# Kernel optimization log

Measured on AMD Instinct MI355X. Metric: run time of the kernel, lower is better.

## Reference

```python
import jax, jax.numpy as jnp
import numpy as np

N_QUBITS = 10
Q_DEPTH = 6


def _apply_1q(state, gate, wire):
    """Apply a 2x2 gate (or batched [B,2,2] gates) to `wire` of state [B,2,...,2]."""
    s = jnp.moveaxis(state, wire + 1, -1)
    if gate.ndim == 2:
        s = s @ gate.T  # new_j = sum_i G[j,i] * old_i
    else:
        s = jnp.einsum('b...i,bji->b...j', s, gate)
    return jnp.moveaxis(s, -1, wire + 1)


def _apply_cnot(state, ctrl, tgt):
    s = jnp.moveaxis(state, (ctrl + 1, tgt + 1), (-2, -1))
    s = jnp.stack([s[..., 0, :], s[..., 1, ::-1]], axis=-2)  # flip target where ctrl=1
    return jnp.moveaxis(s, (-2, -1), (ctrl + 1, tgt + 1))


def _ry(theta):
    """RY(theta) = [[cos(t/2), -sin(t/2)], [sin(t/2), cos(t/2)]]; theta scalar or [B]."""
    c, s = jnp.cos(theta / 2.0), jnp.sin(theta / 2.0)
    return jnp.stack([jnp.stack([c, -s], -1), jnp.stack([s, c], -1)], -2)


def _vqc(angles, q_weights):
    """angles: [B, n_qubits] per-sample RY angles; q_weights: [q_depth, n_qubits].
    Returns <PauliZ_w> for every wire: [B, n_qubits]. All gates are real -> float32 state."""
    B, n = angles.shape
    q_depth = q_weights.shape[0]
    # H-layer on |0...0> gives the uniform superposition: all amplitudes 2^{-n/2}
    state = jnp.full((B,) + (2,) * n, 2.0 ** (-n / 2.0), dtype=angles.dtype)
    # RY layer with per-sample input angles
    for w in range(n):
        state = _apply_1q(state, _ry(angles[:, w]), w)
    # q_depth x (brick-wall CNOT entangler + trainable RY layer)
    for k in range(q_depth):
        for i in range(0, n - 1, 2):
            state = _apply_cnot(state, i, i + 1)
        for i in range(1, n - 1, 2):
            state = _apply_cnot(state, i, i + 1)
        for w in range(n):
            state = _apply_1q(state, _ry(q_weights[k, w]), w)
    # expval(PauliZ(w)) = P(wire w = 0) - P(wire w = 1)
    probs = state * state  # real statevector
    exps = []
    for w in range(n):
        p = jnp.moveaxis(probs, w + 1, 1).reshape(B, 2, -1).sum(-1)
        exps.append(p[:, 0] - p[:, 1])
    return jnp.stack(exps, -1)


def setup_inputs() -> dict:
    key = jax.random.key(0)
    ks = jax.random.split(key, 6)
    B, D_IN, OUT = 8192, 512, 64
    x = jax.random.normal(ks[0], (B, D_IN), dtype=jnp.float32)
    W1 = jax.random.normal(ks[1], (D_IN, N_QUBITS), dtype=jnp.float32) * (1.0 / np.sqrt(D_IN))
    b1 = jnp.zeros((N_QUBITS,), dtype=jnp.float32)
    # keras 'uniform' initializer: U(-0.05, 0.05)
    q_weights = jax.random.uniform(ks[2], (Q_DEPTH, N_QUBITS), dtype=jnp.float32,
                                   minval=-0.05, maxval=0.05)
    W2 = jax.random.normal(ks[3], (N_QUBITS, OUT), dtype=jnp.float32) * (1.0 / np.sqrt(N_QUBITS))
    b2 = jnp.zeros((OUT,), dtype=jnp.float32)
    return {"x": x, "W1": W1, "b1": b1, "q_weights": q_weights, "W2": W2, "b2": b2}


def reference(x, W1, b1, q_weights, W2, b2):
    # Dense(n_qubits, tanh) then scale to angles in (-pi/2, pi/2)
    angles = jnp.tanh(x @ W1 + b1) * (jnp.pi / 2.0)  # [B, n_qubits]
    q_out = _vqc(angles, q_weights)                   # [B, n_qubits]
    return q_out @ W2 + b2                            # [B, output_dim]
```

## Files before the change

### kernel.cpp

```cpp
#include <hip/hip_runtime.h>

#define NQ 10
#define QD 6
#define DIN 512
#define DOUT 64

typedef float v2f __attribute__((ext_vector_type(2)));

__device__ __forceinline__ v2f sp(float s) { v2f r; r.x = s; r.y = s; return r; }
__device__ __forceinline__ v2f mk(float a, float b) { v2f r; r.x = a; r.y = b; return r; }
#define PKF(a, b, c) __builtin_elementwise_fma(a, b, c)

template <int CTRL>
__device__ __forceinline__ float dppf(float v) {
    return __int_as_float(__builtin_amdgcn_mov_dpp(__float_as_int(v), CTRL, 0xF, 0xF, true));
}
template <int M>
__device__ __forceinline__ float sx(float v) {
    if constexpr (M == 1)       return dppf<0xB1>(v);
    else if constexpr (M == 2)  return dppf<0x4E>(v);
    else if constexpr (M == 4)  return dppf<0x1B>(dppf<0x141>(v));
    else if constexpr (M == 8)  return dppf<0x128>(v);
    else return __int_as_float(__builtin_amdgcn_ds_swizzle(__float_as_int(v), 0x401F));
}
template <int M>
__device__ __forceinline__ v2f sx2(v2f v) { return mk(sx<M>(v.x), sx<M>(v.y)); }
__device__ __forceinline__ float red32(float v) {
    v += dppf<0x128>(v);
    v += dppf<0x124>(v);
    v += dppf<0x122>(v);
    v += dppf<0x121>(v);
    v += sx<16>(v);
    return v;
}

__global__ __launch_bounds__(256, 4) void dqc_main(
    const float* __restrict__ x,
    const float* __restrict__ W1,
    const float* __restrict__ b1,
    const float* __restrict__ qw,
    const float* __restrict__ W2,
    const float* __restrict__ b2,
    float* __restrict__ out,
    const int B)
{
    __shared__ __align__(16) float csl[2 * QD * NQ];

    const int tid = threadIdx.x;
    if (tid < QD * NQ) {
        float s, c;
        sincosf(qw[tid] * 0.5f, &s, &c);
        csl[2 * tid] = c; csl[2 * tid + 1] = s;
    }

    const int lane32 = tid & 31;
    const int b  = (blockIdx.x * 256 + tid) >> 5;
    const int bb = (b < B) ? b : (B - 1);

    float xr[16];
    {
        const float4* xp = (const float4*)(x + (size_t)bb * DIN + lane32 * 16);
        #pragma unroll
        for (int i = 0; i < 4; ++i) {
            const float4 v = xp[i];
            xr[4*i] = v.x; xr[4*i+1] = v.y; xr[4*i+2] = v.z; xr[4*i+3] = v.w;
        }
    }
    float dot[NQ];
    #pragma unroll
    for (int w = 0; w < NQ; ++w) dot[w] = 0.f;
    {
        const float4* wp = (const float4*)(W1 + (size_t)lane32 * 16 * NQ);
        #pragma unroll
        for (int j = 0; j < 8; ++j) {
            const float4 f0 = wp[5*j], f1 = wp[5*j+1], f2 = wp[5*j+2],
                         f3 = wp[5*j+3], f4 = wp[5*j+4];
            const float xa = xr[2*j], xb = xr[2*j+1];
            dot[0]=fmaf(xa,f0.x,dot[0]); dot[1]=fmaf(xa,f0.y,dot[1]);
            dot[2]=fmaf(xa,f0.z,dot[2]); dot[3]=fmaf(xa,f0.w,dot[3]);
            dot[4]=fmaf(xa,f1.x,dot[4]); dot[5]=fmaf(xa,f1.y,dot[5]);
            dot[6]=fmaf(xa,f1.z,dot[6]); dot[7]=fmaf(xa,f1.w,dot[7]);
            dot[8]=fmaf(xa,f2.x,dot[8]); dot[9]=fmaf(xa,f2.y,dot[9]);
            dot[0]=fmaf(xb,f2.z,dot[0]); dot[1]=fmaf(xb,f2.w,dot[1]);
            dot[2]=fmaf(xb,f3.x,dot[2]); dot[3]=fmaf(xb,f3.y,dot[3]);
            dot[4]=fmaf(xb,f3.z,dot[4]); dot[5]=fmaf(xb,f3.w,dot[5]);
            dot[6]=fmaf(xb,f4.x,dot[6]); dot[7]=fmaf(xb,f4.y,dot[7]);
            dot[8]=fmaf(xb,f4.z,dot[8]); dot[9]=fmaf(xb,f4.w,dot[9]);
        }
    }
    #pragma unroll
    for (int w = 0; w < NQ; ++w) dot[w] = red32(dot[w]);

    float u0[NQ], u1[NQ];
    #pragma unroll
    for (int w = 0; w < NQ; ++w) {
        const float th2 = tanhf(dot[w] + b1[w]) * 0.78539816339744830962f;
        float s, c;
        sincosf(th2, &s, &c);
        const float isq2 = 0.70710678118654752440f;
        u0[w] = (c - s) * isq2;
        u1[w] = (c + s) * isq2;
    }

    v2f A[16];
    {
        float lf = ((lane32 & 16) ? u1[0] : u0[0]);
        lf *= ((((lane32 >> 3) ^ (lane32 >> 4)) & 1) ? u1[1] : u0[1]);
        lf *= ((lane32 & 4) ? u1[2] : u0[2]);
        lf *= ((((lane32 >> 1) ^ (lane32 >> 2)) & 1) ? u1[3] : u0[3]);
        lf *= ((lane32 & 1) ? u1[4] : u0[4]);
        const bool b0 = (lane32 & 1) != 0;
        const float w5a = b0 ? u1[5] : u0[5];
        const float w5b = b0 ? u0[5] : u1[5];
        #pragma unroll
        for (int m = 0; m < 16; ++m) {
            float f = ((m & 8) ? w5b : w5a);
            f *= ((m & 4) ? u1[6] : u0[6]);
            f *= ((((m >> 1) ^ (m >> 2)) & 1) ? u1[7] : u0[7]);
            f *= ((m & 1) ? u1[8] : u0[8]);
            f *= lf;
            A[m] = (m & 1) ? mk(f * u1[9], f * u0[9]) : mk(f * u0[9], f * u1[9]);
        }
    }

    __syncthreads();

    #pragma unroll 1
    for (int k = 0; k < QD; ++k) {
        const float4* cp = (const float4*)(csl + k * 2 * NQ);
        const float4 g0 = cp[0], g1 = cp[1], g2 = cp[2], g3 = cp[3], g4 = cp[4];
        const float C0=g0.x,S0=g0.y, C1=g0.z,S1=g0.w;
        const float C2=g1.x,S2=g1.y, C3=g1.z,S3=g1.w;
        const float C4=g2.x,S4=g2.y, C5=g2.z,S5=g2.w;
        const float C6=g3.x,S6=g3.y, C7=g3.z,S7=g3.w;
        const float C8=g4.x,S8=g4.y, C9=g4.z,S9=g4.w;
        const bool fuse = (k < QD - 1);

        {
            const float g = (lane32 & 16) ? S0 : -S0;
            const v2f al = sp(C0), be = sp(g);
            #pragma unroll
            for (int m = 0; m < 16; ++m) { const v2f p = sx2<16>(A[m]); A[m] = PKF(al, A[m], be * p); }
        }
        {
            const float g = (lane32 & 4) ? S2 : -S2;
            const bool cb = (lane32 & 8) != 0;
            const v2f al = sp(cb ? g : C2), be = sp(cb ? C2 : g);
            #pragma unroll
            for (int m = 0; m < 16; ++m) { const v2f p = sx2<4>(A[m]); A[m] = PKF(al, A[m], be * p); }
        }
        {
            const float g = (lane32 & 1) ? S4 : -S4;
            const bool cb = (lane32 & 2) != 0;
            const v2f al = sp(cb ? g : C4), be = sp(cb ? C4 : g);
            #pragma unroll
            for (int m = 0; m < 16; ++m) { const v2f p = sx2<1>(A[m]); A[m] = PKF(al, A[m], be * p); }
        }
        {
            #pragma unroll
            for (int m = 0; m < 16; ++m) {
                if (m & 4) continue;
                const v2f lo = A[m], hi = A[m + 4];
                if ((m >> 3) & 1) {
                    A[m]     = PKF(sp(-S6), lo, sp(C6) * hi);
                    A[m + 4] = PKF(sp( S6), hi, sp(C6) * lo);
                } else {
                    A[m]     = PKF(sp(C6), lo, sp(-S6) * hi);
                    A[m + 4] = PKF(sp(C6), hi, sp( S6) * lo);
                }
            }
        }
        {
            #pragma unroll
            for (int m = 0; m < 16; m += 2) {
                const v2f lo = A[m], hi = A[m + 1];
                if ((m >> 1) & 1) {
                    A[m]     = PKF(sp(-S8), lo, sp(C8) * hi);
                    A[m + 1] = PKF(sp( S8), hi, sp(C8) * lo);
                } else {
                    A[m]     = PKF(sp(C8), lo, sp(-S8) * hi);
                    A[m + 1] = PKF(sp(C8), hi, sp( S8) * lo);
                }
            }
        }

        {
            const float g = (lane32 & 8) ? S1 : -S1;
            const bool cb = fuse && ((lane32 & 16) != 0);
            const v2f al = sp(cb ? -g : C1), be = sp(cb ? C1 : g);
            #pragma unroll
            for (int m = 0; m < 16; ++m) { const v2f p = sx2<8>(A[m]); A[m] = PKF(al, A[m], be * p); }
        }
        {
            const float g = (lane32 & 2) ? S3 : -S3;
            const bool cb = fuse && ((lane32 & 4) != 0);
            const v2f al = sp(cb ? -g : C3), be = sp(cb ? C3 : g);
            #pragma unroll
            for (int m = 0; m < 16; ++m) { const v2f p = sx2<2>(A[m]); A[m] = PKF(al, A[m], be * p); }
        }
        {
            const bool cb = fuse && ((lane32 & 1) != 0);
            const v2f a_lo = sp(cb ?  S5 : C5), b_lo = sp(cb ? C5 : -S5);
            const v2f a_hi = sp(cb ? -S5 : C5), b_hi = sp(cb ? C5 :  S5);
            #pragma unroll
            for (int m = 0; m < 8; ++m) {
                const v2f lo = A[m], hi = A[m + 8];
                A[m]     = PKF(a_lo, lo, b_lo * hi);
                A[m + 8] = PKF(a_hi, hi, b_hi * lo);
            }
        }
        {
            #pragma unroll
            for (int m = 0; m < 16; ++m) {
                if (m & 2) continue;
                const v2f lo = A[m], hi = A[m + 2];
                if (fuse && ((m >> 2) & 1)) {
                    A[m]     = PKF(sp( S7), lo, sp(C7) * hi);
                    A[m + 2] = PKF(sp(-S7), hi, sp(C7) * lo);
                } else {
                    A[m]     = PKF(sp(C7), lo, sp(-S7) * hi);
                    A[m + 2] = PKF(sp(C7), hi, sp( S7) * lo);
                }
            }
        }
        {
            const v2f Ae = sp(C9), Be = mk(-S9, S9);
            const v2f Ao = fuse ? mk(S9, -S9) : Ae;
            const v2f Bo = fuse ? sp(C9) : Be;
            #pragma unroll
            for (int m = 0; m < 16; ++m) {
                const v2f s = mk(A[m].y, A[m].x);
                A[m] = (m & 1) ? PKF(Ao, A[m], Bo * s) : PKF(Ae, A[m], Be * s);
            }
        }
    }

    v2f tot2 = sp(0.f), q5 = sp(0.f), q6 = sp(0.f), q7 = sp(0.f), q8 = sp(0.f);
    #pragma unroll
    for (int m = 0; m < 16; ++m) {
        const v2f P = A[m] * A[m];
        tot2 += P;
        if (m & 8) q5 += P;
        if (m & 4) q6 += P;
        if (m & 2) q7 += P;
        if (m & 1) q8 += P;
    }
    const float tot = tot2.x + tot2.y;
    float e[NQ];
    e[0] = (lane32 & 16) ? -tot : tot;
    e[1] = (lane32 & 8)  ? -tot : tot;
    e[2] = (lane32 & 4)  ? -tot : tot;
    e[3] = (lane32 & 2)  ? -tot : tot;
    e[4] = (lane32 & 1)  ? -tot : tot;
    e[5] = tot - 2.f * (q5.x + q5.y);
    e[6] = tot - 2.f * (q6.x + q6.y);
    e[7] = tot - 2.f * (q7.x + q7.y);
    e[8] = tot - 2.f * (q8.x + q8.y);
    e[9] = tot - 2.f * tot2.y;
    #pragma unroll
    for (int w = 0; w < NQ; ++w) e[w] = red32(e[w]);

    if (b < B) {
        float2 o = ((const float2*)b2)[lane32];
        #pragma unroll
        for (int w = 0; w < NQ; ++w) {
            const float2 wv = ((const float2*)(W2 + w * DOUT))[lane32];
            o.x = fmaf(e[w], wv.x, o.x);
            o.y = fmaf(e[w], wv.y, o.y);
        }
        ((float2*)(out + (size_t)b * DOUT))[lane32] = o;
    }
}

extern "C" void kernel_launch(void* const* d_in, const int* in_sizes, int n_in,
                              void* d_out, int out_size, void* d_ws, size_t ws_size,
                              hipStream_t stream) {
    const float* x  = (const float*)d_in[0];
    const float* W1 = (const float*)d_in[1];
    const float* b1 = (const float*)d_in[2];
    const float* qw = (const float*)d_in[3];
    const float* W2 = (const float*)d_in[4];
    const float* b2 = (const float*)d_in[5];
    float* out = (float*)d_out;

    const int B = in_sizes[0] / DIN;
    const int blocks = (B + 7) / 8;
    dqc_main<<<blocks, 256, 0, stream>>>(x, W1, b1, qw, W2, b2, out, B);
}
```

Measured before the change: 108.6 us.

## Spread each sample's statevector across a full 64-lane wavefront instead of 32 lanes

Each sample's 1024-amplitude state now spans 64 lanes with 8 packed pairs per lane instead of 32 lanes with 16 pairs. Wire 0 swaps across the half-wavefront through ds_bpermute, and reductions gain a cross-half step. Gate constants are regrouped in shared memory into even and odd wire sets. The change also uses inline-asm packed FMA/mul/add and doubles the occupancy hint in launch bounds. It halves per-lane register state and work to raise parallelism, at the cost of an LDS-based permute for one wire, a longer reduction and more blocks.

```diff
diff --git a/kernel.cpp b/kernel.cpp
--- a/kernel.cpp
+++ b/kernel.cpp
@@ -9,7 +9,16 @@
 
 __device__ __forceinline__ v2f sp(float s) { v2f r; r.x = s; r.y = s; return r; }
 __device__ __forceinline__ v2f mk(float a, float b) { v2f r; r.x = a; r.y = b; return r; }
-#define PKF(a, b, c) __builtin_elementwise_fma(a, b, c)
+
+__device__ __forceinline__ v2f pk_fma(v2f a, v2f b, v2f c) {
+    v2f d; asm("v_pk_fma_f32 %0, %1, %2, %3" : "=v"(d) : "v"(a), "v"(b), "v"(c)); return d;
+}
+__device__ __forceinline__ v2f pk_mul(v2f a, v2f b) {
+    v2f d; asm("v_pk_mul_f32 %0, %1, %2" : "=v"(d) : "v"(a), "v"(b)); return d;
+}
+__device__ __forceinline__ v2f pk_add(v2f a, v2f b) {
+    v2f d; asm("v_pk_add_f32 %0, %1, %2" : "=v"(d) : "v"(a), "v"(b)); return d;
+}
 
 template <int CTRL>
 __device__ __forceinline__ float dppf(float v) {
@@ -21,20 +30,24 @@
     else if constexpr (M == 2)  return dppf<0x4E>(v);
     else if constexpr (M == 4)  return dppf<0x1B>(dppf<0x141>(v));
     else if constexpr (M == 8)  return dppf<0x128>(v);
-    else return __int_as_float(__builtin_amdgcn_ds_swizzle(__float_as_int(v), 0x401F));
+    else                        return __int_as_float(__builtin_amdgcn_ds_swizzle(__float_as_int(v), 0x401F));
+}
+__device__ __forceinline__ float sx32(float v, int xaddr) {
+    return __int_as_float(__builtin_amdgcn_ds_bpermute(xaddr, __float_as_int(v)));
 }
 template <int M>
 __device__ __forceinline__ v2f sx2(v2f v) { return mk(sx<M>(v.x), sx<M>(v.y)); }
-__device__ __forceinline__ float red32(float v) {
+__device__ __forceinline__ float red64(float v, int xaddr) {
     v += dppf<0x128>(v);
     v += dppf<0x124>(v);
     v += dppf<0x122>(v);
     v += dppf<0x121>(v);
-    v += sx<16>(v);
+    v += __int_as_float(__builtin_amdgcn_ds_swizzle(__float_as_int(v), 0x401F));
+    v += sx32(v, xaddr);
     return v;
 }
 
-__global__ __launch_bounds__(256, 4) void dqc_main(
+__global__ __launch_bounds__(256, 8) void dqc_main(
     const float* __restrict__ x,
     const float* __restrict__ W1,
     const float* __restrict__ b1,
@@ -44,35 +57,36 @@
     float* __restrict__ out,
     const int B)
 {
-    __shared__ __align__(16) float csl[2 * QD * NQ];
+    __shared__ __align__(16) float csl[QD * 24];
 
     const int tid = threadIdx.x;
     if (tid < QD * NQ) {
+        const int layer = tid / NQ, wire = tid - layer * NQ;
         float s, c;
         sincosf(qw[tid] * 0.5f, &s, &c);
-        csl[2 * tid] = c; csl[2 * tid + 1] = s;
-    }
-
-    const int lane32 = tid & 31;
-    const int b  = (blockIdx.x * 256 + tid) >> 5;
+        const int pos = layer * 24 + (wire & 1) * 12 + (wire >> 1) * 2;
+        csl[pos] = c; csl[pos + 1] = s;
+    }
+
+    const int lane = tid & 63;
+    const int b = blockIdx.x * 4 + (tid >> 6);
     const int bb = (b < B) ? b : (B - 1);
-
-    float xr[16];
+    const int xaddr = ((tid ^ 32) & 63) << 2;
+
+    float xr[8];
     {
-        const float4* xp = (const float4*)(x + (size_t)bb * DIN + lane32 * 16);
-        #pragma unroll
-        for (int i = 0; i < 4; ++i) {
-            const float4 v = xp[i];
-            xr[4*i] = v.x; xr[4*i+1] = v.y; xr[4*i+2] = v.z; xr[4*i+3] = v.w;
-        }
+        const float4* xp = (const float4*)(x + (size_t)bb * DIN + lane * 8);
+        const float4 v0 = xp[0], v1 = xp[1];
+        xr[0]=v0.x; xr[1]=v0.y; xr[2]=v0.z; xr[3]=v0.w;
+        xr[4]=v1.x; xr[5]=v1.y; xr[6]=v1.z; xr[7]=v1.w;
     }
     float dot[NQ];
     #pragma unroll
     for (int w = 0; w < NQ; ++w) dot[w] = 0.f;
     {
-        const float4* wp = (const float4*)(W1 + (size_t)lane32 * 16 * NQ);
+        const float4* wp = (const float4*)(W1 + (size_t)lane * 8 * NQ);
         #pragma unroll
-        for (int j = 0; j < 8; ++j) {
+        for (int j = 0; j < 4; ++j) {
             const float4 f0 = wp[5*j], f1 = wp[5*j+1], f2 = wp[5*j+2],
                          f3 = wp[5*j+3], f4 = wp[5*j+4];
             const float xa = xr[2*j], xb = xr[2*j+1];
@@ -89,7 +103,7 @@
         }
     }
     #pragma unroll
-    for (int w = 0; w < NQ; ++w) dot[w] = red32(dot[w]);
+    for (int w = 0; w < NQ; ++w) dot[w] = red64(dot[w], xaddr);
 
     float u0[NQ], u1[NQ];
     #pragma unroll
@@ -102,20 +116,17 @@
         u1[w] = (c + s) * isq2;
     }
 
-    v2f A[16];
+    v2f A[8];
     {
-        float lf = ((lane32 & 16) ? u1[0] : u0[0]);
-        lf *= ((((lane32 >> 3) ^ (lane32 >> 4)) & 1) ? u1[1] : u0[1]);
-        lf *= ((lane32 & 4) ? u1[2] : u0[2]);
-        lf *= ((((lane32 >> 1) ^ (lane32 >> 2)) & 1) ? u1[3] : u0[3]);
-        lf *= ((lane32 & 1) ? u1[4] : u0[4]);
-        const bool b0 = (lane32 & 1) != 0;
-        const float w5a = b0 ? u1[5] : u0[5];
-        const float w5b = b0 ? u0[5] : u1[5];
+        float lf = ((lane & 32) ? u1[0] : u0[0]);
+        lf *= ((((lane >> 4) ^ (lane >> 5)) & 1) ? u1[1] : u0[1]);
+        lf *= ((lane & 8) ? u1[2] : u0[2]);
+        lf *= ((((lane >> 2) ^ (lane >> 3)) & 1) ? u1[3] : u0[3]);
+        lf *= ((lane & 2) ? u1[4] : u0[4]);
+        lf *= (((lane ^ (lane >> 1)) & 1) ? u1[5] : u0[5]);
         #pragma unroll
-        for (int m = 0; m < 16; ++m) {
-            float f = ((m & 8) ? w5b : w5a);
-            f *= ((m & 4) ? u1[6] : u0[6]);
+        for (int m = 0; m < 8; ++m) {
+            float f = ((m & 4) ? u1[6] : u0[6]);
             f *= ((((m >> 1) ^ (m >> 2)) & 1) ? u1[7] : u0[7]);
             f *= ((m & 1) ? u1[8] : u0[8]);
             f *= lf;
@@ -127,148 +138,170 @@
 
     #pragma unroll 1
     for (int k = 0; k < QD; ++k) {
-        const float4* cp = (const float4*)(csl + k * 2 * NQ);
-        const float4 g0 = cp[0], g1 = cp[1], g2 = cp[2], g3 = cp[3], g4 = cp[4];
-        const float C0=g0.x,S0=g0.y, C1=g0.z,S1=g0.w;
-        const float C2=g1.x,S2=g1.y, C3=g1.z,S3=g1.w;
-        const float C4=g2.x,S4=g2.y, C5=g2.z,S5=g2.w;
-        const float C6=g3.x,S6=g3.y, C7=g3.z,S7=g3.w;
-        const float C8=g4.x,S8=g4.y, C9=g4.z,S9=g4.w;
-        const bool fuse = (k < QD - 1);
-
-        {
-            const float g = (lane32 & 16) ? S0 : -S0;
-            const v2f al = sp(C0), be = sp(g);
-            #pragma unroll
-            for (int m = 0; m < 16; ++m) { const v2f p = sx2<16>(A[m]); A[m] = PKF(al, A[m], be * p); }
-        }
-        {
-            const float g = (lane32 & 4) ? S2 : -S2;
-            const bool cb = (lane32 & 8) != 0;
-            const v2f al = sp(cb ? g : C2), be = sp(cb ? C2 : g);
-            #pragma unroll
-            for (int m = 0; m < 16; ++m) { const v2f p = sx2<4>(A[m]); A[m] = PKF(al, A[m], be * p); }
-        }
-        {
-            const float g = (lane32 & 1) ? S4 : -S4;
-            const bool cb = (lane32 & 2) != 0;
-            const v2f al = sp(cb ? g : C4), be = sp(cb ? C4 : g);
-            #pragma unroll
-            for (int m = 0; m < 16; ++m) { const v2f p = sx2<1>(A[m]); A[m] = PKF(al, A[m], be * p); }
-        }
-        {
-            #pragma unroll
-            for (int m = 0; m < 16; ++m) {
-                if (m & 4) continue;
+        const float* ce = csl + k * 24;
+        const bool fuse = (k != QD - 1);
+
+        const float4 ea = *(const float4*)(ce);
+        const float4 eb = *(const float4*)(ce + 4);
+        const float2 ec = *(const float2*)(ce + 8);
+        const float C0=ea.x, S0=ea.y, C2=ea.z, S2=ea.w;
+        const float C4=eb.x, S4=eb.y, C6=eb.z, S6=eb.w;
+        const float C8=ec.x, S8=ec.y;
+
+        {
+            const float g = (lane & 32) ? S0 : -S0;
+            const v2f alv = sp(C0), bev = sp(g);
+            #pragma unroll
+            for (int m = 0; m < 8; ++m) {
+                const v2f p = mk(sx32(A[m].x, xaddr), sx32(A[m].y, xaddr));
+                A[m] = pk_fma(alv, A[m], pk_mul(bev, p));
+            }
+        }
+        {
+            const float g = (lane & 8) ? S2 : -S2;
+            const bool cb = (lane & 16) != 0;
+            const v2f alv = sp(cb ? g : C2), bev = sp(cb ? C2 : g);
+            #pragma unroll
+            for (int m = 0; m < 8; ++m) {
+                const v2f p = sx2<8>(A[m]);
+                A[m] = pk_fma(alv, A[m], pk_mul(bev, p));
+            }
+        }
+        {
+            const float g = (lane & 2) ? S4 : -S4;
+            const bool cb = (lane & 4) != 0;
+            const v2f alv = sp(cb ? g : C4), bev = sp(cb ? C4 : g);
+            #pragma unroll
+            for (int m = 0; m < 8; ++m) {
+                const v2f p = sx2<2>(A[m]);
+                A[m] = pk_fma(alv, A[m], pk_mul(bev, p));
+            }
+        }
+        {
+            const bool cb = (lane & 1) != 0;
+            const v2f a_lo = sp(cb ? -S6 : C6), b_lo = sp(cb ? C6 : -S6);
+            const v2f a_hi = sp(cb ?  S6 : C6), b_hi = sp(cb ? C6 :  S6);
+            #pragma unroll
+            for (int m = 0; m < 4; ++m) {
                 const v2f lo = A[m], hi = A[m + 4];
-                if ((m >> 3) & 1) {
-                    A[m]     = PKF(sp(-S6), lo, sp(C6) * hi);
-                    A[m + 4] = PKF(sp( S6), hi, sp(C6) * lo);
+                A[m]     = pk_fma(a_lo, lo, pk_mul(b_lo, hi));
+                A[m + 4] = pk_fma(a_hi, hi, pk_mul(b_hi, lo));
+            }
+        }
+        {
+            const v2f c8 = sp(C8), s8 = sp(S8), ns8 = sp(-S8);
+            #pragma unroll
+            for (int m = 0; m < 8; m += 2) {
+                const v2f lo = A[m], hi = A[m + 1];
+                if (m & 2) {
+                    A[m]     = pk_fma(ns8, lo, pk_mul(c8, hi));
+                    A[m + 1] = pk_fma(s8,  hi, pk_mul(c8, lo));
                 } else {
-                    A[m]     = PKF(sp(C6), lo, sp(-S6) * hi);
-                    A[m + 4] = PKF(sp(C6), hi, sp( S6) * lo);
+                    A[m]     = pk_fma(c8, lo, pk_mul(ns8, hi));
+                    A[m + 1] = pk_fma(c8, hi, pk_mul(s8,  lo));
                 }
             }
         }
-        {
-            #pragma unroll
-            for (int m = 0; m < 16; m += 2) {
-                const v2f lo = A[m], hi = A[m + 1];
-                if ((m >> 1) & 1) {
-                    A[m]     = PKF(sp(-S8), lo, sp(C8) * hi);
-                    A[m + 1] = PKF(sp( S8), hi, sp(C8) * lo);
+
+        const float4 oa = *(const float4*)(ce + 12);
+        const float4 ob = *(const float4*)(ce + 16);
+        const float2 oc = *(const float2*)(ce + 20);
+        const float C1=oa.x, S1=oa.y, C3=oa.z, S3=oa.w;
+        const float C5=ob.x, S5=ob.y, C7=ob.z, S7=ob.w;
+        const float C9=oc.x, S9=oc.y;
+
+        {
+            const float g = (lane & 16) ? S1 : -S1;
+            const bool cb = fuse && ((lane & 32) != 0);
+            const v2f alv = sp(cb ? -g : C1), bev = sp(cb ? C1 : g);
+            #pragma unroll
+            for (int m = 0; m < 8; ++m) {
+                const v2f p = sx2<16>(A[m]);
+                A[m] = pk_fma(alv, A[m], pk_mul(bev, p));
+            }
+        }
+        {
+            const float g = (lane & 4) ? S3 : -S3;
+            const bool cb = fuse && ((lane & 8) != 0);
+            const v2f alv = sp(cb ? -g : C3), bev = sp(cb ? C3 : g);
+            #pragma unroll
+            for (int m = 0; m < 8; ++m) {
+                const v2f p = sx2<4>(A[m]);
+                A[m] = pk_fma(alv, A[m], pk_mul(bev, p));
+            }
+        }
+        {
+            const float g = (lane & 1) ? S5 : -S5;
+            const bool cb = fuse && ((lane & 2) != 0);
+            const v2f alv = sp(cb ? -g : C5), bev = sp(cb ? C5 : g);
+            #pragma unroll
+            for (int m = 0; m < 8; ++m) {
+                const v2f p = sx2<1>(A[m]);
+                A[m] = pk_fma(alv, A[m], pk_mul(bev, p));
+            }
+        }
+        {
+            const v2f c7 = sp(C7), s7 = sp(S7), ns7 = sp(-S7);
+            const v2f a_lo4 = fuse ? s7 : c7,  b_lo4 = fuse ? c7 : ns7;
+            const v2f a_hi4 = fuse ? ns7 : c7, b_hi4 = fuse ? c7 : s7;
+            #pragma unroll
+            for (int m = 0; m < 2; ++m) {
+                {   const v2f lo = A[m], hi = A[m + 2];
+                    A[m]     = pk_fma(c7, lo, pk_mul(ns7, hi));
+                    A[m + 2] = pk_fma(c7, hi, pk_mul(s7,  lo)); }
+                {   const v2f lo = A[m + 4], hi = A[m + 6];
+                    A[m + 4] = pk_fma(a_lo4, lo, pk_mul(b_lo4, hi));
+                    A[m + 6] = pk_fma(a_hi4, hi, pk_mul(b_hi4, lo)); }
+            }
+        }
+        {
+            const float nS9 = -S9;
+            const float axx = fuse ? S9 : C9,  axy = fuse ? C9 : nS9;
+            const float ayy = fuse ? nS9 : C9, ayx = fuse ? C9 : S9;
+            #pragma unroll
+            for (int m = 0; m < 8; ++m) {
+                const float ax = A[m].x, ay = A[m].y;
+                if (m & 1) {
+                    A[m].x = fmaf(axx, ax, axy * ay);
+                    A[m].y = fmaf(ayy, ay, ayx * ax);
                 } else {
-                    A[m]     = PKF(sp(C8), lo, sp(-S8) * hi);
-                    A[m + 1] = PKF(sp(C8), hi, sp( S8) * lo);
+                    A[m].x = fmaf(C9, ax, nS9 * ay);
+                    A[m].y = fmaf(C9, ay, S9  * ax);
                 }
             }
         }
-
-        {
-            const float g = (lane32 & 8) ? S1 : -S1;
-            const bool cb = fuse && ((lane32 & 16) != 0);
-            const v2f al = sp(cb ? -g : C1), be = sp(cb ? C1 : g);
-            #pragma unroll
-            for (int m = 0; m < 16; ++m) { const v2f p = sx2<8>(A[m]); A[m] = PKF(al, A[m], be * p); }
-        }
-        {
-            const float g = (lane32 & 2) ? S3 : -S3;
-            const bool cb = fuse && ((lane32 & 4) != 0);
-            const v2f al = sp(cb ? -g : C3), be = sp(cb ? C3 : g);
-            #pragma unroll
-            for (int m = 0; m < 16; ++m) { const v2f p = sx2<2>(A[m]); A[m] = PKF(al, A[m], be * p); }
-        }
-        {
-            const bool cb = fuse && ((lane32 & 1) != 0);
-            const v2f a_lo = sp(cb ?  S5 : C5), b_lo = sp(cb ? C5 : -S5);
-            const v2f a_hi = sp(cb ? -S5 : C5), b_hi = sp(cb ? C5 :  S5);
-            #pragma unroll
-            for (int m = 0; m < 8; ++m) {
-                const v2f lo = A[m], hi = A[m + 8];
-                A[m]     = PKF(a_lo, lo, b_lo * hi);
-                A[m + 8] = PKF(a_hi, hi, b_hi * lo);
-            }
-        }
-        {
-            #pragma unroll
-            for (int m = 0; m < 16; ++m) {
-                if (m & 2) continue;
-                const v2f lo = A[m], hi = A[m + 2];
-                if (fuse && ((m >> 2) & 1)) {
-                    A[m]     = PKF(sp( S7), lo, sp(C7) * hi);
-                    A[m + 2] = PKF(sp(-S7), hi, sp(C7) * lo);
-                } else {
-                    A[m]     = PKF(sp(C7), lo, sp(-S7) * hi);
-                    A[m + 2] = PKF(sp(C7), hi, sp( S7) * lo);
-                }
-            }
-        }
-        {
-            const v2f Ae = sp(C9), Be = mk(-S9, S9);
-            const v2f Ao = fuse ? mk(S9, -S9) : Ae;
-            const v2f Bo = fuse ? sp(C9) : Be;
-            #pragma unroll
-            for (int m = 0; m < 16; ++m) {
-                const v2f s = mk(A[m].y, A[m].x);
-                A[m] = (m & 1) ? PKF(Ao, A[m], Bo * s) : PKF(Ae, A[m], Be * s);
-            }
-        }
-    }
-
-    v2f tot2 = sp(0.f), q5 = sp(0.f), q6 = sp(0.f), q7 = sp(0.f), q8 = sp(0.f);
-    #pragma unroll
-    for (int m = 0; m < 16; ++m) {
-        const v2f P = A[m] * A[m];
-        tot2 += P;
-        if (m & 8) q5 += P;
-        if (m & 4) q6 += P;
-        if (m & 2) q7 += P;
-        if (m & 1) q8 += P;
-    }
+    }
+
+    v2f P[8];
+    #pragma unroll
+    for (int m = 0; m < 8; ++m) P[m] = pk_mul(A[m], A[m]);
+    const v2f s01 = pk_add(P[0], P[1]), s23 = pk_add(P[2], P[3]);
+    const v2f s45 = pk_add(P[4], P[5]), s67 = pk_add(P[6], P[7]);
+    const v2f q8v = pk_add(pk_add(P[1], P[3]), pk_add(P[5], P[7]));
+    const v2f q6v = pk_add(s45, s67);
+    const v2f q7v = pk_add(s23, s67);
+    const v2f tot2 = pk_add(pk_add(s01, s23), q6v);
     const float tot = tot2.x + tot2.y;
+
     float e[NQ];
-    e[0] = (lane32 & 16) ? -tot : tot;
-    e[1] = (lane32 & 8)  ? -tot : tot;
-    e[2] = (lane32 & 4)  ? -tot : tot;
-    e[3] = (lane32 & 2)  ? -tot : tot;
-    e[4] = (lane32 & 1)  ? -tot : tot;
-    e[5] = tot - 2.f * (q5.x + q5.y);
-    e[6] = tot - 2.f * (q6.x + q6.y);
-    e[7] = tot - 2.f * (q7.x + q7.y);
-    e[8] = tot - 2.f * (q8.x + q8.y);
-    e[9] = tot - 2.f * tot2.y;
-    #pragma unroll
-    for (int w = 0; w < NQ; ++w) e[w] = red32(e[w]);
+    e[0] = (lane & 32) ? -tot : tot;
+    e[1] = (lane & 16) ? -tot : tot;
+    e[2] = (lane & 8)  ? -tot : tot;
+    e[3] = (lane & 4)  ? -tot : tot;
+    e[4] = (lane & 2)  ? -tot : tot;
+    e[5] = (lane & 1)  ? -tot : tot;
+    e[6] = fmaf(-2.f, q6v.x + q6v.y, tot);
+    e[7] = fmaf(-2.f, q7v.x + q7v.y, tot);
+    e[8] = fmaf(-2.f, q8v.x + q8v.y, tot);
+    e[9] = fmaf(-2.f, tot2.y, tot);
+    #pragma unroll
+    for (int w = 0; w < NQ; ++w) e[w] = red64(e[w], xaddr);
 
     if (b < B) {
-        float2 o = ((const float2*)b2)[lane32];
+        float o = b2[lane];
         #pragma unroll
-        for (int w = 0; w < NQ; ++w) {
-            const float2 wv = ((const float2*)(W2 + w * DOUT))[lane32];
-            o.x = fmaf(e[w], wv.x, o.x);
-            o.y = fmaf(e[w], wv.y, o.y);
-        }
-        ((float2*)(out + (size_t)b * DOUT))[lane32] = o;
+        for (int w = 0; w < NQ; ++w) o = fmaf(e[w], W2[w * DOUT + lane], o);
+        out[(size_t)b * DOUT + lane] = o;
     }
 }
 
@@ -284,6 +317,6 @@
     float* out = (float*)d_out;
 
     const int B = in_sizes[0] / DIN;
-    const int blocks = (B + 7) / 8;
+    const int blocks = (B + 3) / 4;
     dqc_main<<<blocks, 256, 0, stream>>>(x, W1, b1, qw, W2, b2, out, B);
 }
```

Result: faster. 106.2 us (-2.2%).
